# Kernel optimization log

Measured on AMD Instinct MI355X. Metric: run time of the kernel, lower is better.

Reference implementation:

```python
import jax, jax.numpy as jnp
import numpy as np

QD = 512        # query_dim == key_dim
SD = 64         # spa_embed_dim
K = 4           # num_attn heads
EPS = 1e-6      # LayerNorm eps (space2vec LayerNorm)
SLOPE = 0.01    # nn.LeakyReLU default negative_slope


def setup_inputs() -> dict:
    key = jax.random.key(0)
    ks = jax.random.split(key, 6)
    B, N = 4096, 32
    D = 2 * QD + SD  # concat dim when have_query_embed=True
    xav = (6.0 / (D + K)) ** 0.5
    return {
        "key_embeds": jax.random.normal(ks[0], (B, N, QD), dtype=jnp.float32),
        "key_spa_embeds": jax.random.normal(ks[1], (B, N, SD), dtype=jnp.float32),
        "query_embed": jax.random.normal(ks[2], (B, QD), dtype=jnp.float32),
        "atten_vecs": jax.random.uniform(ks[3], (D, K), minval=-xav, maxval=xav, dtype=jnp.float32),
        "post_w": jax.random.normal(ks[4], (QD, QD), dtype=jnp.float32) * 0.02,
        "post_b": jnp.zeros((QD,), dtype=jnp.float32),
        "pre_ln_g": jnp.ones((QD,), dtype=jnp.float32),
        "pre_ln_b": jnp.zeros((QD,), dtype=jnp.float32),
        "post_ln_g": jnp.ones((QD,), dtype=jnp.float32),
        "post_ln_b": jnp.zeros((QD,), dtype=jnp.float32),
    }


def _layernorm(x, g, b):
    m = jnp.mean(x, axis=-1, keepdims=True)
    v = jnp.mean((x - m) ** 2, axis=-1, keepdims=True)
    return g * (x - m) / jnp.sqrt(v + EPS) + b


def reference(key_embeds, key_spa_embeds, query_embed, atten_vecs,
              post_w, post_b, pre_ln_g, pre_ln_b, post_ln_g, post_ln_b):
    B, N, _ = key_embeds.shape
    # expand query over context points and concat: [B, N, 2*QD+SD]
    q_exp = jnp.broadcast_to(query_embed[:, None, :], (B, N, QD))
    concat = jnp.concatenate([q_exp, key_embeds, key_spa_embeds], axis=2)
    # attention logits per head: [B, N, K]
    attn = jnp.einsum('bnd,dk->bnk', concat, atten_vecs)
    attn = jax.nn.leaky_relu(attn, SLOPE)
    attn = jax.nn.softmax(attn, axis=1)  # softmax over context points
    # weighted sum per head, then average over heads: [B, QD]
    combined = jnp.einsum('bnk,bnd->bkd', attn, key_embeds).sum(axis=1) * (1.0 / K)
    combined = jax.nn.sigmoid(combined)
    # pre layernorm with residual from query
    combined = _layernorm(combined + query_embed, pre_ln_g, pre_ln_b)
    # post linear (dropout in eval mode = identity) + residual + post LN
    lin = combined @ post_w.T + post_b
    out = _layernorm(lin + combined, post_ln_g, post_ln_b)
    return out
```

## Files before the change

### kernel.cpp

```cpp
#include <hip/hip_runtime.h>
#include <hip/hip_bf16.h>

#define QD 512
#define SD 64
#define NCTX 32
#define ROWA 1088
#define ROWB 1152
#define ABUF (NCTX * ROWA)

constexpr float EPS_LN = 1e-6f;
constexpr float SLOPE = 0.01f;

typedef __attribute__((ext_vector_type(8))) __bf16 bf16x8;
typedef __attribute__((ext_vector_type(4))) float f32x4;

__device__ __forceinline__ float red64(float v) {
#pragma unroll
    for (int m = 32; m; m >>= 1) v += __shfl_xor(v, m, 64);
    return v;
}

__device__ __forceinline__ float b2f(unsigned short u) {
    unsigned int x = ((unsigned int)u) << 16;
    return __builtin_bit_cast(float, x);
}
__device__ __forceinline__ unsigned short f2bu(float f) {
    __hip_bfloat16 h = __float2bfloat16(f);
    return __builtin_bit_cast(unsigned short, h);
}

__device__ __forceinline__ bf16x8 pack8(float4 a, float4 b) {
    bf16x8 r;
    r[0] = (__bf16)a.x; r[1] = (__bf16)a.y; r[2] = (__bf16)a.z; r[3] = (__bf16)a.w;
    r[4] = (__bf16)b.x; r[5] = (__bf16)b.y; r[6] = (__bf16)b.z; r[7] = (__bf16)b.w;
    return r;
}

struct SpFrag { float4 a0, b0, a1, b1; };

__device__ __forceinline__ void load_pass(const float* kb, int wave, int lane,
                                          int pass, float4 kr[8]) {
#pragma unroll
    for (int i = 0; i < 4; ++i) {
        const float* krow = kb + (8 * wave + 4 * pass + i) * QD;
        kr[2 * i]     = reinterpret_cast<const float4*>(krow)[2 * lane];
        kr[2 * i + 1] = reinterpret_cast<const float4*>(krow)[2 * lane + 1];
    }
}
__device__ __forceinline__ void write_pass(unsigned char* sA, int wave, int lane,
                                           int pass, const float4 kr[8]) {
#pragma unroll
    for (int i = 0; i < 4; ++i) {
        const int n = 8 * wave + 4 * pass + i;
        *reinterpret_cast<bf16x8*>(&sA[n * ROWA + 16 * lane]) =
            pack8(kr[2 * i], kr[2 * i + 1]);
    }
}
__device__ __forceinline__ SpFrag load_sp(const float* sb, int wave, int lane) {
    SpFrag s;
    s.a0 = s.b0 = s.a1 = s.b1 = make_float4(0.f, 0.f, 0.f, 0.f);
    if (wave < 2) {
        const int arow = 16 * wave + (lane & 15);
        const int qq8 = (lane >> 4) * 8;
        const float* s0p = sb + arow * SD + qq8;
        const float* s1p = sb + arow * SD + 32 + qq8;
        s.a0 = reinterpret_cast<const float4*>(s0p)[0];
        s.b0 = reinterpret_cast<const float4*>(s0p)[1];
        s.a1 = reinterpret_cast<const float4*>(s1p)[0];
        s.b1 = reinterpret_cast<const float4*>(s1p)[1];
    }
    return s;
}
__device__ __forceinline__ void ql_compute(const float* qb, const float4* av4,
                                           float* dst, int lane) {
    const float4* q4 = reinterpret_cast<const float4*>(qb);
    float s0 = 0.f, s1 = 0.f, s2 = 0.f, s3 = 0.f;
#pragma unroll
    for (int h = 0; h < 2; ++h) {
        const float4 qv = q4[2 * lane + h];
        const float4 a0 = av4[8 * lane + 4 * h + 0];
        const float4 a1 = av4[8 * lane + 4 * h + 1];
        const float4 a2 = av4[8 * lane + 4 * h + 2];
        const float4 a3 = av4[8 * lane + 4 * h + 3];
        s0 += qv.x * a0.x + qv.y * a1.x + qv.z * a2.x + qv.w * a3.x;
        s1 += qv.x * a0.y + qv.y * a1.y + qv.z * a2.y + qv.w * a3.y;
        s2 += qv.x * a0.z + qv.y * a1.z + qv.z * a2.z + qv.w * a3.z;
        s3 += qv.x * a0.w + qv.y * a1.w + qv.z * a2.w + qv.w * a3.w;
    }
    s0 = red64(s0); s1 = red64(s1); s2 = red64(s2); s3 = red64(s3);
    if (lane == 0) { dst[0] = s0; dst[1] = s1; dst[2] = s2; dst[3] = s3; }
}

__device__ __forceinline__ void mfma_phase(
    const unsigned char* sA, const unsigned char* sB, const SpFrag& sp,
    const float* ql4, float (*s_logit)[4], int wave, int lane)
{
    if (wave >= 2) return;
    const int colB = lane & 15;
    const int kgrp = (lane >> 4) * 16;
    const int arow = 16 * wave + (lane & 15);
    f32x4 acc = {0.f, 0.f, 0.f, 0.f};
    bf16x8 bz;
#pragma unroll
    for (int e = 0; e < 8; ++e) bz[e] = (__bf16)0.0f;
#pragma unroll
    for (int ks = 0; ks < 16; ++ks) {
        const int koff = ks * 64 + kgrp;
        const bf16x8 af =
            *reinterpret_cast<const bf16x8*>(&sA[arow * ROWA + koff]);
        bf16x8 bf = bz;
        if (colB < 4)
            bf = *reinterpret_cast<const bf16x8*>(
                &sB[colB * ROWB + (koff ^ (colB << 4))]);
        acc = __builtin_amdgcn_mfma_f32_16x16x32_bf16(af, bf, acc, 0, 0, 0);
    }
#pragma unroll
    for (int ks = 0; ks < 2; ++ks) {
        const int koff = 1024 + ks * 64 + kgrp;
        const bf16x8 af = (ks == 0) ? pack8(sp.a0, sp.b0) : pack8(sp.a1, sp.b1);
        bf16x8 bf = bz;
        if (colB < 4)
            bf = *reinterpret_cast<const bf16x8*>(
                &sB[colB * ROWB + (koff ^ (colB << 4))]);
        acc = __builtin_amdgcn_mfma_f32_16x16x32_bf16(af, bf, acc, 0, 0, 0);
    }
    if (colB < 4) {
        const float qlk = ql4[colB];
#pragma unroll
        for (int r = 0; r < 4; ++r) {
            const int row = 16 * wave + (lane >> 4) * 4 + r;
            float v = acc[r] + qlk;
            v = v > 0.f ? v : SLOPE * v;
            s_logit[row][colB] = v;
        }
    }
}

__device__ __forceinline__ void softmax_phase(
    float (*s_logit)[4], float* s_w, int wave, int lane)
{
    if (wave != 0) return;
    const int n = lane & 31;
    float v0 = s_logit[n][0], v1 = s_logit[n][1],
          v2 = s_logit[n][2], v3 = s_logit[n][3];
    float m0 = v0, m1 = v1, m2 = v2, m3 = v3;
#pragma unroll
    for (int m = 16; m; m >>= 1) {
        m0 = fmaxf(m0, __shfl_xor(m0, m, 32));
        m1 = fmaxf(m1, __shfl_xor(m1, m, 32));
        m2 = fmaxf(m2, __shfl_xor(m2, m, 32));
        m3 = fmaxf(m3, __shfl_xor(m3, m, 32));
    }
    float e0 = __expf(v0 - m0), e1 = __expf(v1 - m1),
          e2 = __expf(v2 - m2), e3 = __expf(v3 - m3);
    float st0 = e0, st1 = e1, st2 = e2, st3 = e3;
#pragma unroll
    for (int m = 16; m; m >>= 1) {
        st0 += __shfl_xor(st0, m, 32);
        st1 += __shfl_xor(st1, m, 32);
        st2 += __shfl_xor(st2, m, 32);
        st3 += __shfl_xor(st3, m, 32);
    }
    const float w = 0.25f * (e0 / st0 + e1 / st1 + e2 / st2 + e3 / st3);
    if (lane < 32) s_w[n] = w;
}

__device__ __forceinline__ void wsum_phase(
    const unsigned char* sA, const float* s_w, const float* qb,
    const float* lng, const float* lnb, float* yrow,
    float* s_red, int wave, int lane, int t)
{
    const int d0 = 2 * t;
    float acc0 = 0.f, acc1 = 0.f;
#pragma unroll
    for (int n = 0; n < NCTX; ++n) {
        const float wn = s_w[n];
        const unsigned int u =
            *reinterpret_cast<const unsigned int*>(&sA[n * ROWA + 4 * t]);
        acc0 += wn * b2f((unsigned short)(u & 0xffffu));
        acc1 += wn * b2f((unsigned short)(u >> 16));
    }
    const float2 qv = *reinterpret_cast<const float2*>(&qb[d0]);
    const float x0 = 1.f / (1.f + __expf(-acc0)) + qv.x;
    const float x1 = 1.f / (1.f + __expf(-acc1)) + qv.y;

    float sum = red64(x0 + x1);
    float ssq = red64(x0 * x0 + x1 * x1);
    if (lane == 0) { s_red[wave] = sum; s_red[4 + wave] = ssq; }
    __syncthreads();
    sum = s_red[0] + s_red[1] + s_red[2] + s_red[3];
    ssq = s_red[4] + s_red[5] + s_red[6] + s_red[7];
    const float mean = sum * (1.f / QD);
    const float var = ssq * (1.f / QD) - mean * mean;
    const float inv = rsqrtf(var + EPS_LN);
    const float2 gg = *reinterpret_cast<const float2*>(&lng[d0]);
    const float2 bb = *reinterpret_cast<const float2*>(&lnb[d0]);
    float2 o;
    o.x = gg.x * (x0 - mean) * inv + bb.x;
    o.y = gg.y * (x1 - mean) * inv + bb.y;
    *reinterpret_cast<float2*>(&yrow[d0]) = o;
}

__global__ __launch_bounds__(256, 2) void attn_fuse(
    const float* __restrict__ key, const float* __restrict__ spa,
    const float* __restrict__ query, const float* __restrict__ av,
    const float* __restrict__ lng, const float* __restrict__ lnb,
    float* __restrict__ yout,
    const float* __restrict__ postw, unsigned short* __restrict__ wb16)
{
    __shared__ __align__(16) unsigned char s_A[2 * ABUF];
    __shared__ __align__(16) unsigned char s_B[4 * ROWB];
    __shared__ float s_logit[NCTX][4];
    __shared__ float s_w[NCTX];
    __shared__ float s_red[8];
    __shared__ float s_ql[2][4];

    const int g = blockIdx.x;
    const int b0 = 2 * g, b1 = 2 * g + 1;
    const int t = threadIdx.x;
    const int wave = t >> 6;
    const int lane = t & 63;

    const float* kb0 = key + (size_t)b0 * (NCTX * QD);
    const float* kb1 = key + (size_t)b1 * (NCTX * QD);
    const float* qb0 = query + (size_t)b0 * QD;
    const float* qb1 = query + (size_t)b1 * QD;
    const float* sb0 = spa + (size_t)b0 * (NCTX * SD);
    const float* sb1 = spa + (size_t)b1 * (NCTX * SD);
    const float4* av4 = reinterpret_cast<const float4*>(av);
    unsigned char* sA0 = s_A;
    unsigned char* sA1 = s_A + ABUF;

    if (t < 32) {
        const int idx = g * 32 + t;
        const float4 wv = reinterpret_cast<const float4*>(postw)[idx];
        ushort4 h;
        h.x = f2bu(wv.x); h.y = f2bu(wv.y); h.z = f2bu(wv.z); h.w = f2bu(wv.w);
        reinterpret_cast<ushort4*>(wb16)[idx] = h;
    }

    {
        float4 kr[8];
        load_pass(kb0, wave, lane, 0, kr); write_pass(sA0, wave, lane, 0, kr);
        load_pass(kb0, wave, lane, 1, kr); write_pass(sA0, wave, lane, 1, kr);
    }
    SpFrag spc = load_sp(sb0, wave, lane);
    {
        float avreg[9];
#pragma unroll
        for (int r = 0; r < 9; ++r)
            avreg[r] = av[(size_t)(512 + lane * 9 + r) * 4 + wave];
#pragma unroll
        for (int r = 0; r < 9; ++r) {
            const int k = lane * 9 + r;
            *reinterpret_cast<__bf16*>(
                &s_B[wave * ROWB + ((2 * k) ^ (wave << 4))]) = (__bf16)avreg[r];
        }
    }
    if (wave == 3) ql_compute(qb0, av4, s_ql[0], lane);
    __syncthreads();

    float4 p0[8];
    load_pass(kb1, wave, lane, 0, p0);
    SpFrag spn = load_sp(sb1, wave, lane);
    if (wave == 3) ql_compute(qb1, av4, s_ql[1], lane);
    mfma_phase(sA0, s_B, spc, s_ql[0], s_logit, wave, lane);
    __syncthreads();

    write_pass(sA1, wave, lane, 0, p0);
    float4 p1[8];
    load_pass(kb1, wave, lane, 1, p1);
    softmax_phase(s_logit, s_w, wave, lane);
    __syncthreads();

    wsum_phase(sA0, s_w, qb0, lng, lnb, yout + (size_t)b0 * QD,
               s_red, wave, lane, t);
    write_pass(sA1, wave, lane, 1, p1);
    __syncthreads();

    mfma_phase(sA1, s_B, spn, s_ql[1], s_logit, wave, lane);
    __syncthreads();
    softmax_phase(s_logit, s_w, wave, lane);
    __syncthreads();
    wsum_phase(sA1, s_w, qb1, lng, lnb, yout + (size_t)b1 * QD,
               s_red, wave, lane, t);
}

__device__ __forceinline__ int swzB(int row, int off) {
    return row * 128 + (off ^ ((row & 7) << 4));
}

__global__ __launch_bounds__(256) void post_gemm(
    const float* __restrict__ Y, const unsigned short* __restrict__ Wb,
    const float* __restrict__ pbias, float* __restrict__ out)
{
    __shared__ __align__(16) unsigned char Ys[64 * 128];
    __shared__ __align__(16) unsigned char Ws[64 * 128];
    const int t = threadIdx.x;
    const int wave = t >> 6, lane = t & 63;
    const int bm = blockIdx.x * 64;
    const int bn = blockIdx.y * 64;

    const int lr = t >> 2;
    const int lq = (t & 3) * 16;

    f32x4 acc[4] = {{0.f,0.f,0.f,0.f},{0.f,0.f,0.f,0.f},
                    {0.f,0.f,0.f,0.f},{0.f,0.f,0.f,0.f}};

    for (int kc = 0; kc < QD; kc += 64) {
        float4 ya[4];
        const float* yrow = Y + (size_t)(bm + lr) * QD + kc + lq;
        const unsigned short* wrow = Wb + (size_t)(bn + lr) * QD + kc + lq;
#pragma unroll
        for (int j = 0; j < 4; ++j)
            ya[j] = reinterpret_cast<const float4*>(yrow)[j];
        const uint4 wa = reinterpret_cast<const uint4*>(wrow)[0];
        const uint4 wb = reinterpret_cast<const uint4*>(wrow)[1];
        __syncthreads();
        const int base = lq * 2;
        *reinterpret_cast<bf16x8*>(&Ys[swzB(lr, base)])      = pack8(ya[0], ya[1]);
        *reinterpret_cast<bf16x8*>(&Ys[swzB(lr, base + 16)]) = pack8(ya[2], ya[3]);
        *reinterpret_cast<uint4*>(&Ws[swzB(lr, base)])       = wa;
        *reinterpret_cast<uint4*>(&Ws[swzB(lr, base + 16)])  = wb;
        __syncthreads();
#pragma unroll
        for (int ks = 0; ks < 2; ++ks) {
            const int ko = ks * 64 + (lane >> 4) * 16;
            const bf16x8 af = *reinterpret_cast<const bf16x8*>(
                &Ys[swzB(16 * wave + (lane & 15), ko)]);
#pragma unroll
            for (int c = 0; c < 4; ++c) {
                const bf16x8 bf = *reinterpret_cast<const bf16x8*>(
                    &Ws[swzB(16 * c + (lane & 15), ko)]);
                acc[c] = __builtin_amdgcn_mfma_f32_16x16x32_bf16(af, bf, acc[c],
                                                                 0, 0, 0);
            }
        }
    }
    const int m0 = bm + 16 * wave + (lane >> 4) * 4;
#pragma unroll
    for (int c = 0; c < 4; ++c) {
        const int n = bn + 16 * c + (lane & 15);
        const float pb = pbias[n];
#pragma unroll
        for (int r = 0; r < 4; ++r) {
            const size_t idx = (size_t)(m0 + r) * QD + n;
            out[idx] = acc[c][r] + pb + Y[idx];
        }
    }
}

__global__ __launch_bounds__(256) void post_ln_kernel(
    float* __restrict__ out,
    const float* __restrict__ lng, const float* __restrict__ lnb)
{
    __shared__ float s_red[8];
    const int r = blockIdx.x;
    const int t = threadIdx.x;
    const int wave = t >> 6, lane = t & 63;
    const int d0 = 2 * t;
    const float2 lv = *reinterpret_cast<const float2*>(&out[(size_t)r * QD + d0]);
    const float x0 = lv.x;
    const float x1 = lv.y;
    float sum = red64(x0 + x1);
    float ssq = red64(x0 * x0 + x1 * x1);
    if (lane == 0) { s_red[wave] = sum; s_red[4 + wave] = ssq; }
    __syncthreads();
    sum = s_red[0] + s_red[1] + s_red[2] + s_red[3];
    ssq = s_red[4] + s_red[5] + s_red[6] + s_red[7];
    const float mean = sum * (1.f / QD);
    const float var = ssq * (1.f / QD) - mean * mean;
    const float inv = rsqrtf(var + EPS_LN);
    const float2 gg = *reinterpret_cast<const float2*>(&lng[d0]);
    const float2 bb = *reinterpret_cast<const float2*>(&lnb[d0]);
    float2 o;
    o.x = gg.x * (x0 - mean) * inv + bb.x;
    o.y = gg.y * (x1 - mean) * inv + bb.y;
    *reinterpret_cast<float2*>(&out[(size_t)r * QD + d0]) = o;
}

extern "C" void kernel_launch(void* const* d_in, const int* in_sizes, int n_in,
                              void* d_out, int out_size, void* d_ws, size_t ws_size,
                              hipStream_t stream) {
    const float* key    = (const float*)d_in[0];
    const float* spa    = (const float*)d_in[1];
    const float* query  = (const float*)d_in[2];
    const float* av     = (const float*)d_in[3];
    const float* postw  = (const float*)d_in[4];
    const float* postb  = (const float*)d_in[5];
    const float* pre_g  = (const float*)d_in[6];
    const float* pre_b  = (const float*)d_in[7];
    const float* post_g = (const float*)d_in[8];
    const float* post_b = (const float*)d_in[9];
    float* out = (float*)d_out;
    float* yws = (float*)d_ws;
    unsigned short* wb16 =
        (unsigned short*)((char*)d_ws + (8u << 20));

    const int B = in_sizes[2] / QD;

    attn_fuse<<<B / 2, 256, 0, stream>>>(key, spa, query, av, pre_g, pre_b,
                                         yws, postw, wb16);
    dim3 gridB(B / 64, QD / 64);
    post_gemm<<<gridB, 256, 0, stream>>>(yws, wb16, postb, out);
    post_ln_kernel<<<B, 256, 0, stream>>>(out, post_g, post_b);
}
```

Before: 88.08 us.

## Single-buffer key tile in LDS with XOR swizzle to raise occupancy

Drops the double-buffered LDS tile for the key rows and keeps one swizzled buffer. The second batch's key data is held in registers until the first batch's weighted sum finishes, with an extra barrier before it is written. Halving LDS use lets launch bounds go from 2 to 4 blocks per CU, and the XOR swizzle on row offsets is meant to cut LDS bank conflicts. The cost is less overlap between loading the second batch and computing the first, plus more live registers (p0, p1 and spn) under a tighter register budget, which risks spills.

```diff
diff --git a/kernel.cpp b/kernel.cpp
--- a/kernel.cpp
+++ b/kernel.cpp
@@ -6,7 +6,6 @@
 #define NCTX 32
 #define ROWA 1088
 #define ROWB 1152
-#define ABUF (NCTX * ROWA)
 
 constexpr float EPS_LN = 1e-6f;
 constexpr float SLOPE = 0.01f;
@@ -27,6 +26,10 @@
 __device__ __forceinline__ unsigned short f2bu(float f) {
     __hip_bfloat16 h = __float2bfloat16(f);
     return __builtin_bit_cast(unsigned short, h);
+}
+
+__device__ __forceinline__ int swz(int row, int off) {
+    return row * ROWA + (off ^ ((row & 7) << 4));
 }
 
 __device__ __forceinline__ bf16x8 pack8(float4 a, float4 b) {
@@ -52,7 +55,7 @@
 #pragma unroll
     for (int i = 0; i < 4; ++i) {
         const int n = 8 * wave + 4 * pass + i;
-        *reinterpret_cast<bf16x8*>(&sA[n * ROWA + 16 * lane]) =
+        *reinterpret_cast<bf16x8*>(&sA[swz(n, 16 * lane)]) =
             pack8(kr[2 * i], kr[2 * i + 1]);
     }
 }
@@ -98,7 +101,7 @@
     if (wave >= 2) return;
     const int colB = lane & 15;
     const int kgrp = (lane >> 4) * 16;
-    const int arow = 16 * wave + (lane & 15);
+    const int arow = 16 * wave + colB;
     f32x4 acc = {0.f, 0.f, 0.f, 0.f};
     bf16x8 bz;
 #pragma unroll
@@ -107,7 +110,7 @@
     for (int ks = 0; ks < 16; ++ks) {
         const int koff = ks * 64 + kgrp;
         const bf16x8 af =
-            *reinterpret_cast<const bf16x8*>(&sA[arow * ROWA + koff]);
+            *reinterpret_cast<const bf16x8*>(&sA[swz(arow, koff)]);
         bf16x8 bf = bz;
         if (colB < 4)
             bf = *reinterpret_cast<const bf16x8*>(
@@ -176,7 +179,7 @@
     for (int n = 0; n < NCTX; ++n) {
         const float wn = s_w[n];
         const unsigned int u =
-            *reinterpret_cast<const unsigned int*>(&sA[n * ROWA + 4 * t]);
+            *reinterpret_cast<const unsigned int*>(&sA[swz(n, 4 * t)]);
         acc0 += wn * b2f((unsigned short)(u & 0xffffu));
         acc1 += wn * b2f((unsigned short)(u >> 16));
     }
@@ -201,14 +204,14 @@
     *reinterpret_cast<float2*>(&yrow[d0]) = o;
 }
 
-__global__ __launch_bounds__(256, 2) void attn_fuse(
+__global__ __launch_bounds__(256, 4) void attn_fuse(
     const float* __restrict__ key, const float* __restrict__ spa,
     const float* __restrict__ query, const float* __restrict__ av,
     const float* __restrict__ lng, const float* __restrict__ lnb,
     float* __restrict__ yout,
     const float* __restrict__ postw, unsigned short* __restrict__ wb16)
 {
-    __shared__ __align__(16) unsigned char s_A[2 * ABUF];
+    __shared__ __align__(16) unsigned char s_A[NCTX * ROWA];
     __shared__ __align__(16) unsigned char s_B[4 * ROWB];
     __shared__ float s_logit[NCTX][4];
     __shared__ float s_w[NCTX];
@@ -228,8 +231,6 @@
     const float* sb0 = spa + (size_t)b0 * (NCTX * SD);
     const float* sb1 = spa + (size_t)b1 * (NCTX * SD);
     const float4* av4 = reinterpret_cast<const float4*>(av);
-    unsigned char* sA0 = s_A;
-    unsigned char* sA1 = s_A + ABUF;
 
     if (t < 32) {
         const int idx = g * 32 + t;
@@ -241,8 +242,8 @@
 
     {
         float4 kr[8];
-        load_pass(kb0, wave, lane, 0, kr); write_pass(sA0, wave, lane, 0, kr);
-        load_pass(kb0, wave, lane, 1, kr); write_pass(sA0, wave, lane, 1, kr);
+        load_pass(kb0, wave, lane, 0, kr); write_pass(s_A, wave, lane, 0, kr);
+        load_pass(kb0, wave, lane, 1, kr); write_pass(s_A, wave, lane, 1, kr);
     }
     SpFrag spc = load_sp(sb0, wave, lane);
     {
@@ -262,27 +263,29 @@
 
     float4 p0[8];
     load_pass(kb1, wave, lane, 0, p0);
-    SpFrag spn = load_sp(sb1, wave, lane);
     if (wave == 3) ql_compute(qb1, av4, s_ql[1], lane);
-    mfma_phase(sA0, s_B, spc, s_ql[0], s_logit, wave, lane);
-    __syncthreads();
-
-    write_pass(sA1, wave, lane, 0, p0);
+    mfma_phase(s_A, s_B, spc, s_ql[0], s_logit, wave, lane);
+    __syncthreads();
+
     float4 p1[8];
     load_pass(kb1, wave, lane, 1, p1);
+    SpFrag spn = load_sp(sb1, wave, lane);
     softmax_phase(s_logit, s_w, wave, lane);
     __syncthreads();
 
-    wsum_phase(sA0, s_w, qb0, lng, lnb, yout + (size_t)b0 * QD,
+    wsum_phase(s_A, s_w, qb0, lng, lnb, yout + (size_t)b0 * QD,
                s_red, wave, lane, t);
-    write_pass(sA1, wave, lane, 1, p1);
-    __syncthreads();
-
-    mfma_phase(sA1, s_B, spn, s_ql[1], s_logit, wave, lane);
+    __syncthreads();
+
+    write_pass(s_A, wave, lane, 0, p0);
+    write_pass(s_A, wave, lane, 1, p1);
+    __syncthreads();
+
+    mfma_phase(s_A, s_B, spn, s_ql[1], s_logit, wave, lane);
     __syncthreads();
     softmax_phase(s_logit, s_w, wave, lane);
     __syncthreads();
-    wsum_phase(sA1, s_w, qb1, lng, lnb, yout + (size_t)b1 * QD,
+    wsum_phase(s_A, s_w, qb1, lng, lnb, yout + (size_t)b1 * QD,
                s_red, wave, lane, t);
 }
 
@@ -402,6 +405,6 @@
     attn_fuse<<<B / 2, 256, 0, stream>>>(key, spa, query, av, pre_g, pre_b,
                                          yws, postw, wb16);
     dim3 gridB(B / 64, QD / 64);
-    post_gemm<<<gridB, 256, 0, stream>>>(yws, wb16, postb, out);
+    post_gemm<<<gridB, 64 * 4, 0, stream>>>(yws, wb16, postb, out);
     post_ln_kernel<<<B, 256, 0, stream>>>(out, post_g, post_b);
 }
```

Result: slower. 93.88 us (+6.6%).
